# Kernel optimization log

Hardware: AMD Instinct MI355X
Metric: run time of the kernel (lower is better)

Reference implementation:

```python
import jax, jax.numpy as jnp
import numpy as np

H = 2048
B, L, S = 4, 4096, 10

def setup_inputs() -> dict:
    key = jax.random.key(0)
    k1, k2, k3, k4, k5, k6 = jax.random.split(key, 6)
    scale = 1.0 / np.sqrt(H)
    return {
        "h_english": jax.random.normal(k1, (B, L, H), dtype=jnp.float32),
        "h_lojban": jax.random.normal(k2, (B, S, H), dtype=jnp.float32),
        "w_q": jax.random.normal(k3, (H, H), dtype=jnp.float32) * scale,
        "w_k": jax.random.normal(k4, (H, H), dtype=jnp.float32) * scale,
        "w_v": jax.random.normal(k5, (H, H), dtype=jnp.float32) * scale,
        "w_o": jax.random.normal(k6, (H, H), dtype=jnp.float32) * scale,
        "alpha": jnp.float32(0.1),
    }

def reference(h_english, h_lojban, w_q, w_k, w_v, w_o, alpha):
    h = h_english.shape[-1]
    # torch Linear: y = x @ W^T
    q = jnp.einsum('blh,oh->blo', h_english, w_q)   # [B,L,H]
    k = jnp.einsum('bsh,oh->bso', h_lojban, w_k)    # [B,S,H]
    v = jnp.einsum('bsh,oh->bso', h_lojban, w_v)    # [B,S,H]
    scores = jnp.einsum('blh,bsh->bls', q, k) / jnp.sqrt(jnp.float32(h))  # [B,L,S]
    probs = jax.nn.softmax(scores, axis=-1)
    context = jnp.einsum('bls,bsh->blh', probs, v)  # [B,L,H]
    delta = jnp.einsum('blh,oh->blo', context, w_o)
    return h_english + alpha * delta
```

## Files before the change

### kernel.cpp

```cpp
#include <hip/hip_runtime.h>

#define SDIM 10
#define HDIM 2048
#define LDIM 4096
#define BDIM 4

#define KSCALE 0.02209708691207961f

__global__ __launch_bounds__(256) void kv_kernel(
    const float* __restrict__ h_l, const float* __restrict__ w_k,
    const float* __restrict__ w_v, float* __restrict__ k_out,
    float* __restrict__ v_out) {
  const int b = blockIdx.y;
  const int wave = threadIdx.x >> 6;
  const int lane = threadIdx.x & 63;
  const int opair = blockIdx.x * 4 + wave;
  const int o0 = opair * 2;

  const float4* hl4 = (const float4*)(h_l + (size_t)b * SDIM * HDIM);
  const float4* wk0 = (const float4*)(w_k + (size_t)o0 * HDIM);
  const float4* wk1 = (const float4*)(w_k + (size_t)(o0 + 1) * HDIM);
  const float4* wv0 = (const float4*)(w_v + (size_t)o0 * HDIM);
  const float4* wv1 = (const float4*)(w_v + (size_t)(o0 + 1) * HDIM);

  float ak0[SDIM], ak1[SDIM], av0[SDIM], av1[SDIM];
#pragma unroll
  for (int s = 0; s < SDIM; s++) { ak0[s] = ak1[s] = av0[s] = av1[s] = 0.f; }

#pragma unroll
  for (int j = 0; j < 8; j++) {
    const int idx = j * 64 + lane;
    const float4 a0 = wk0[idx], a1 = wk1[idx];
    const float4 c0 = wv0[idx], c1 = wv1[idx];
#pragma unroll
    for (int s = 0; s < SDIM; s++) {
      const float4 h = hl4[s * 512 + idx];
      ak0[s] += a0.x * h.x + a0.y * h.y + a0.z * h.z + a0.w * h.w;
      ak1[s] += a1.x * h.x + a1.y * h.y + a1.z * h.z + a1.w * h.w;
      av0[s] += c0.x * h.x + c0.y * h.y + c0.z * h.z + c0.w * h.w;
      av1[s] += c1.x * h.x + c1.y * h.y + c1.z * h.z + c1.w * h.w;
    }
  }
#pragma unroll
  for (int s = 0; s < SDIM; s++) {
#pragma unroll
    for (int d = 1; d < 64; d <<= 1) {
      ak0[s] += __shfl_xor(ak0[s], d);
      ak1[s] += __shfl_xor(ak1[s], d);
      av0[s] += __shfl_xor(av0[s], d);
      av1[s] += __shfl_xor(av1[s], d);
    }
  }
  if (lane == 0) {
#pragma unroll
    for (int s = 0; s < SDIM; s++) {
      const size_t base = ((size_t)b * SDIM + s) * HDIM + o0;
      k_out[base]     = ak0[s];
      k_out[base + 1] = ak1[s];
      v_out[base]     = av0[s];
      v_out[base + 1] = av1[s];
    }
  }
}

#define OSPLIT 16
__global__ __launch_bounds__(256) void kk_part_kernel(
    const float* __restrict__ k_in, const float* __restrict__ w_q,
    float* __restrict__ part) {
  const int b = blockIdx.z;
  const int oc = blockIdx.y >> 1;
  const int s0 = (blockIdx.y & 1) * 5;
  const int f4 = blockIdx.x * 256 + threadIdx.x;

  __shared__ float ksh[5 * 128];
  for (int idx = threadIdx.x; idx < 5 * 128; idx += 256) {
    const int s = idx >> 7, oo = idx & 127;
    ksh[idx] = k_in[((size_t)b * SDIM + s0 + s) * HDIM + oc * 128 + oo];
  }
  __syncthreads();

  float4 acc[5];
#pragma unroll
  for (int s = 0; s < 5; s++) acc[s] = make_float4(0.f, 0.f, 0.f, 0.f);

  const float4* wq4 = (const float4*)w_q;
  for (int oo = 0; oo < 128; oo++) {
    const float4 w = wq4[(size_t)(oc * 128 + oo) * 512 + f4];
#pragma unroll
    for (int s = 0; s < 5; s++) {
      const float kv = ksh[s * 128 + oo];
      acc[s].x += kv * w.x; acc[s].y += kv * w.y;
      acc[s].z += kv * w.z; acc[s].w += kv * w.w;
    }
  }
#pragma unroll
  for (int s = 0; s < 5; s++) {
    ((float4*)part)[(((size_t)oc * BDIM + b) * SDIM + s0 + s) * 512 + f4] = acc[s];
  }
}

__global__ __launch_bounds__(256) void kk_reduce_kernel(
    const float* __restrict__ part, float* __restrict__ kk_out) {
  const int t = blockIdx.x * 256 + threadIdx.x;
  const float4* p4 = (const float4*)part;
  float4 acc = make_float4(0.f, 0.f, 0.f, 0.f);
#pragma unroll
  for (int p = 0; p < OSPLIT; p++) {
    const float4 v = p4[(size_t)p * 20480 + t];
    acc.x += v.x; acc.y += v.y; acc.z += v.z; acc.w += v.w;
  }
  ((float4*)kk_out)[t] = acc;
}

__global__ __launch_bounds__(256) void vo_kernel(
    const float* __restrict__ v_in, const float* __restrict__ w_o,
    float* __restrict__ vo_out) {
  const int b = blockIdx.y;
  const int wave = threadIdx.x >> 6;
  const int lane = threadIdx.x & 63;
  const int opair = blockIdx.x * 4 + wave;
  const int o0 = opair * 2;

  const float4* vb4 = (const float4*)(v_in + (size_t)b * SDIM * HDIM);
  const float4* wo0 = (const float4*)(w_o + (size_t)o0 * HDIM);
  const float4* wo1 = (const float4*)(w_o + (size_t)(o0 + 1) * HDIM);

  float a0[SDIM], a1[SDIM];
#pragma unroll
  for (int s = 0; s < SDIM; s++) { a0[s] = a1[s] = 0.f; }

#pragma unroll
  for (int j = 0; j < 8; j++) {
    const int idx = j * 64 + lane;
    const float4 w0 = wo0[idx], w1 = wo1[idx];
#pragma unroll
    for (int s = 0; s < SDIM; s++) {
      const float4 h = vb4[s * 512 + idx];
      a0[s] += w0.x * h.x + w0.y * h.y + w0.z * h.z + w0.w * h.w;
      a1[s] += w1.x * h.x + w1.y * h.y + w1.z * h.z + w1.w * h.w;
    }
  }
#pragma unroll
  for (int s = 0; s < SDIM; s++) {
#pragma unroll
    for (int d = 1; d < 64; d <<= 1) {
      a0[s] += __shfl_xor(a0[s], d);
      a1[s] += __shfl_xor(a1[s], d);
    }
  }
  if (lane == 0) {
#pragma unroll
    for (int s = 0; s < SDIM; s++) {
      const size_t base = ((size_t)b * SDIM + s) * HDIM + o0;
      vo_out[base]     = a0[s];
      vo_out[base + 1] = a1[s];
    }
  }
}

__global__ __launch_bounds__(256) void attn_kernel(
    const float* __restrict__ h_e, const float* __restrict__ kk,
    const float* __restrict__ vo, const float* __restrict__ alpha_p,
    float* __restrict__ out) {
  const int b = blockIdx.y;
  const int wave = threadIdx.x >> 6;
  const int lane = threadIdx.x & 63;
  const int tid = threadIdx.x;
  const int row0 = blockIdx.x * 8 + wave * 2;
  const float alpha = *alpha_p;
  const float4* kkb = (const float4*)(kk + (size_t)b * SDIM * HDIM);
  const float4* vob = (const float4*)(vo + (size_t)b * SDIM * HDIM);
  const size_t rowbase = ((size_t)b * LDIM + row0) * HDIM;

  __shared__ float4 lds[SDIM * 128];

  float4 he[2][8];
#pragma unroll
  for (int r = 0; r < 2; r++) {
    const float4* src = (const float4*)(h_e + rowbase + (size_t)r * HDIM);
#pragma unroll
    for (int i = 0; i < 8; i++) he[r][i] = src[i * 64 + lane];
  }

  float acc[2][SDIM];
#pragma unroll
  for (int r = 0; r < 2; r++)
#pragma unroll
    for (int s = 0; s < SDIM; s++) acc[r][s] = 0.f;

  float4 st[5];
#pragma unroll
  for (int k = 0; k < 5; k++) {
    const int idx = k * 256 + tid;
    st[k] = kkb[(idx >> 7) * 512 + (idx & 127)];
  }
#pragma unroll
  for (int j = 0; j < 4; j++) {
    __syncthreads();
#pragma unroll
    for (int k = 0; k < 5; k++) lds[k * 256 + tid] = st[k];
    if (j < 3) {
#pragma unroll
      for (int k = 0; k < 5; k++) {
        const int idx = k * 256 + tid;
        st[k] = kkb[(idx >> 7) * 512 + (j + 1) * 128 + (idx & 127)];
      }
    }
    __syncthreads();
#pragma unroll
    for (int ii = 0; ii < 2; ii++) {
      const int i = j * 2 + ii;
#pragma unroll
      for (int s = 0; s < SDIM; s++) {
        const float4 kv = lds[s * 128 + ii * 64 + lane];
#pragma unroll
        for (int r = 0; r < 2; r++)
          acc[r][s] += he[r][i].x * kv.x + he[r][i].y * kv.y +
                       he[r][i].z * kv.z + he[r][i].w * kv.w;
      }
    }
  }

#pragma unroll
  for (int r = 0; r < 2; r++)
#pragma unroll
    for (int s = 0; s < SDIM; s++) {
      float v = acc[r][s];
      v += __shfl_xor(v, 1);
      v += __shfl_xor(v, 2);
      v += __shfl_xor(v, 4);
      v += __shfl_xor(v, 8);
      v += __shfl_xor(v, 16);
      v += __shfl_xor(v, 32);
      acc[r][s] = v * KSCALE;
    }
#pragma unroll
  for (int r = 0; r < 2; r++) {
    float m = acc[r][0];
#pragma unroll
    for (int s = 1; s < SDIM; s++) m = fmaxf(m, acc[r][s]);
    float sum = 0.f;
#pragma unroll
    for (int s = 0; s < SDIM; s++) {
      acc[r][s] = __expf(acc[r][s] - m);
      sum += acc[r][s];
    }
    const float inv = alpha / sum;
#pragma unroll
    for (int s = 0; s < SDIM; s++) acc[r][s] *= inv;
  }

#pragma unroll
  for (int k = 0; k < 5; k++) {
    const int idx = k * 256 + tid;
    st[k] = vob[(idx >> 7) * 512 + (idx & 127)];
  }
#pragma unroll
  for (int j = 0; j < 4; j++) {
    __syncthreads();
#pragma unroll
    for (int k = 0; k < 5; k++) lds[k * 256 + tid] = st[k];
    if (j < 3) {
#pragma unroll
      for (int k = 0; k < 5; k++) {
        const int idx = k * 256 + tid;
        st[k] = vob[(idx >> 7) * 512 + (j + 1) * 128 + (idx & 127)];
      }
    }
    __syncthreads();
#pragma unroll
    for (int ii = 0; ii < 2; ii++) {
      const int i = j * 2 + ii;
      float4 o4[2];
#pragma unroll
      for (int r = 0; r < 2; r++) o4[r] = he[r][i];
#pragma unroll
      for (int s = 0; s < SDIM; s++) {
        const float4 vv = lds[s * 128 + ii * 64 + lane];
#pragma unroll
        for (int r = 0; r < 2; r++) {
          o4[r].x += acc[r][s] * vv.x;
          o4[r].y += acc[r][s] * vv.y;
          o4[r].z += acc[r][s] * vv.z;
          o4[r].w += acc[r][s] * vv.w;
        }
      }
#pragma unroll
      for (int r = 0; r < 2; r++)
        ((float4*)(out + rowbase + (size_t)r * HDIM))[i * 64 + lane] = o4[r];
    }
  }
}

extern "C" void kernel_launch(void* const* d_in, const int* in_sizes, int n_in,
                              void* d_out, int out_size, void* d_ws, size_t ws_size,
                              hipStream_t stream) {
  const float* h_e   = (const float*)d_in[0];
  const float* h_l   = (const float*)d_in[1];
  const float* w_q   = (const float*)d_in[2];
  const float* w_k   = (const float*)d_in[3];
  const float* w_v   = (const float*)d_in[4];
  const float* w_o   = (const float*)d_in[5];
  const float* alpha = (const float*)d_in[6];
  float* out = (float*)d_out;

  float* ws      = (float*)d_ws;
  float* k_ws    = ws;
  float* v_ws    = ws + 81920;
  float* kk_ws   = ws + 163840;
  float* vo_ws   = ws + 245760;
  float* part_ws = ws + 327680;

  kv_kernel<<<dim3(256, BDIM), 256, 0, stream>>>(h_l, w_k, w_v, k_ws, v_ws);
  kk_part_kernel<<<dim3(2, 32, BDIM), 256, 0, stream>>>(k_ws, w_q, part_ws);
  vo_kernel<<<dim3(256, BDIM), 256, 0, stream>>>(v_ws, w_o, vo_ws);
  kk_reduce_kernel<<<80, 256, 0, stream>>>(part_ws, kk_ws);
  attn_kernel<<<dim3(512, BDIM), 256, 0, stream>>>(h_e, kk_ws, vo_ws, alpha, out);
}
```

Before: 454.7 us.

## Stage projection inputs in LDS and async double-buffer attention operands

The K/V and VO projection kernels now launch one block per output slice and loop over the batch inside the block. Each batch's small activation matrix is staged in shared memory, so all batches reading the same weight rows do so close together in time and the weights are more likely to hit in cache. The attention kernel replaces register-staged copies with direct global-to-LDS async loads into a double buffer. This removes one barrier per chunk, and a launch-bounds hint is added to target occupancy. The costs are larger LDS use, less block-level parallelism in the projection kernels, and a reliance on the barrier to wait for the async LDS loads to finish.

```diff
diff --git a/kernel.cpp b/kernel.cpp
--- a/kernel.cpp
+++ b/kernel.cpp
@@ -11,54 +11,60 @@
     const float* __restrict__ h_l, const float* __restrict__ w_k,
     const float* __restrict__ w_v, float* __restrict__ k_out,
     float* __restrict__ v_out) {
-  const int b = blockIdx.y;
   const int wave = threadIdx.x >> 6;
   const int lane = threadIdx.x & 63;
-  const int opair = blockIdx.x * 4 + wave;
-  const int o0 = opair * 2;
-
-  const float4* hl4 = (const float4*)(h_l + (size_t)b * SDIM * HDIM);
+  const int o0 = blockIdx.x * 8 + wave * 2;
+
+  __shared__ float4 hsh[512 * SDIM];
+
   const float4* wk0 = (const float4*)(w_k + (size_t)o0 * HDIM);
   const float4* wk1 = (const float4*)(w_k + (size_t)(o0 + 1) * HDIM);
   const float4* wv0 = (const float4*)(w_v + (size_t)o0 * HDIM);
   const float4* wv1 = (const float4*)(w_v + (size_t)(o0 + 1) * HDIM);
 
-  float ak0[SDIM], ak1[SDIM], av0[SDIM], av1[SDIM];
-#pragma unroll
-  for (int s = 0; s < SDIM; s++) { ak0[s] = ak1[s] = av0[s] = av1[s] = 0.f; }
-
-#pragma unroll
-  for (int j = 0; j < 8; j++) {
-    const int idx = j * 64 + lane;
-    const float4 a0 = wk0[idx], a1 = wk1[idx];
-    const float4 c0 = wv0[idx], c1 = wv1[idx];
+  for (int b = 0; b < BDIM; b++) {
+    __syncthreads();
+    const float4* src = (const float4*)(h_l + (size_t)b * SDIM * HDIM);
+    for (int i = threadIdx.x; i < 512 * SDIM; i += 256) hsh[i] = src[i];
+    __syncthreads();
+
+    float ak0[SDIM], ak1[SDIM], av0[SDIM], av1[SDIM];
+#pragma unroll
+    for (int s = 0; s < SDIM; s++) { ak0[s] = ak1[s] = av0[s] = av1[s] = 0.f; }
+
+#pragma unroll
+    for (int j = 0; j < 8; j++) {
+      const int idx = j * 64 + lane;
+      const float4 a0 = wk0[idx], a1 = wk1[idx];
+      const float4 c0 = wv0[idx], c1 = wv1[idx];
+#pragma unroll
+      for (int s = 0; s < SDIM; s++) {
+        const float4 h = hsh[s * 512 + idx];
+        ak0[s] += a0.x * h.x + a0.y * h.y + a0.z * h.z + a0.w * h.w;
+        ak1[s] += a1.x * h.x + a1.y * h.y + a1.z * h.z + a1.w * h.w;
+        av0[s] += c0.x * h.x + c0.y * h.y + c0.z * h.z + c0.w * h.w;
+        av1[s] += c1.x * h.x + c1.y * h.y + c1.z * h.z + c1.w * h.w;
+      }
+    }
 #pragma unroll
     for (int s = 0; s < SDIM; s++) {
-      const float4 h = hl4[s * 512 + idx];
-      ak0[s] += a0.x * h.x + a0.y * h.y + a0.z * h.z + a0.w * h.w;
-      ak1[s] += a1.x * h.x + a1.y * h.y + a1.z * h.z + a1.w * h.w;
-      av0[s] += c0.x * h.x + c0.y * h.y + c0.z * h.z + c0.w * h.w;
-      av1[s] += c1.x * h.x + c1.y * h.y + c1.z * h.z + c1.w * h.w;
-    }
-  }
-#pragma unroll
-  for (int s = 0; s < SDIM; s++) {
-#pragma unroll
-    for (int d = 1; d < 64; d <<= 1) {
-      ak0[s] += __shfl_xor(ak0[s], d);
-      ak1[s] += __shfl_xor(ak1[s], d);
-      av0[s] += __shfl_xor(av0[s], d);
-      av1[s] += __shfl_xor(av1[s], d);
-    }
-  }
-  if (lane == 0) {
-#pragma unroll
-    for (int s = 0; s < SDIM; s++) {
-      const size_t base = ((size_t)b * SDIM + s) * HDIM + o0;
-      k_out[base]     = ak0[s];
-      k_out[base + 1] = ak1[s];
-      v_out[base]     = av0[s];
-      v_out[base + 1] = av1[s];
+#pragma unroll
+      for (int d = 1; d < 64; d <<= 1) {
+        ak0[s] += __shfl_xor(ak0[s], d);
+        ak1[s] += __shfl_xor(ak1[s], d);
+        av0[s] += __shfl_xor(av0[s], d);
+        av1[s] += __shfl_xor(av1[s], d);
+      }
+    }
+    if (lane == 0) {
+#pragma unroll
+      for (int s = 0; s < SDIM; s++) {
+        const size_t base = ((size_t)b * SDIM + s) * HDIM + o0;
+        k_out[base]     = ak0[s];
+        k_out[base + 1] = ak1[s];
+        v_out[base]     = av0[s];
+        v_out[base + 1] = av1[s];
+      }
     }
   }
 }
@@ -115,50 +121,70 @@
 __global__ __launch_bounds__(256) void vo_kernel(
     const float* __restrict__ v_in, const float* __restrict__ w_o,
     float* __restrict__ vo_out) {
-  const int b = blockIdx.y;
   const int wave = threadIdx.x >> 6;
   const int lane = threadIdx.x & 63;
-  const int opair = blockIdx.x * 4 + wave;
-  const int o0 = opair * 2;
-
-  const float4* vb4 = (const float4*)(v_in + (size_t)b * SDIM * HDIM);
+  const int o0 = blockIdx.x * 8 + wave * 2;
+
+  __shared__ float4 vsh[512 * SDIM];
+
   const float4* wo0 = (const float4*)(w_o + (size_t)o0 * HDIM);
   const float4* wo1 = (const float4*)(w_o + (size_t)(o0 + 1) * HDIM);
 
-  float a0[SDIM], a1[SDIM];
-#pragma unroll
-  for (int s = 0; s < SDIM; s++) { a0[s] = a1[s] = 0.f; }
-
-#pragma unroll
-  for (int j = 0; j < 8; j++) {
-    const int idx = j * 64 + lane;
-    const float4 w0 = wo0[idx], w1 = wo1[idx];
+  for (int b = 0; b < BDIM; b++) {
+    __syncthreads();
+    const float4* src = (const float4*)(v_in + (size_t)b * SDIM * HDIM);
+    for (int i = threadIdx.x; i < 512 * SDIM; i += 256) vsh[i] = src[i];
+    __syncthreads();
+
+    float a0[SDIM], a1[SDIM];
+#pragma unroll
+    for (int s = 0; s < SDIM; s++) { a0[s] = a1[s] = 0.f; }
+
+#pragma unroll
+    for (int j = 0; j < 8; j++) {
+      const int idx = j * 64 + lane;
+      const float4 w0 = wo0[idx], w1 = wo1[idx];
+#pragma unroll
+      for (int s = 0; s < SDIM; s++) {
+        const float4 h = vsh[s * 512 + idx];
+        a0[s] += w0.x * h.x + w0.y * h.y + w0.z * h.z + w0.w * h.w;
+        a1[s] += w1.x * h.x + w1.y * h.y + w1.z * h.z + w1.w * h.w;
+      }
+    }
 #pragma unroll
     for (int s = 0; s < SDIM; s++) {
-      const float4 h = vb4[s * 512 + idx];
-      a0[s] += w0.x * h.x + w0.y * h.y + w0.z * h.z + w0.w * h.w;
-      a1[s] += w1.x * h.x + w1.y * h.y + w1.z * h.z + w1.w * h.w;
-    }
-  }
-#pragma unroll
-  for (int s = 0; s < SDIM; s++) {
-#pragma unroll
-    for (int d = 1; d < 64; d <<= 1) {
-      a0[s] += __shfl_xor(a0[s], d);
-      a1[s] += __shfl_xor(a1[s], d);
-    }
-  }
-  if (lane == 0) {
-#pragma unroll
-    for (int s = 0; s < SDIM; s++) {
-      const size_t base = ((size_t)b * SDIM + s) * HDIM + o0;
-      vo_out[base]     = a0[s];
-      vo_out[base + 1] = a1[s];
-    }
-  }
-}
-
-__global__ __launch_bounds__(256) void attn_kernel(
+#pragma unroll
+      for (int d = 1; d < 64; d <<= 1) {
+        a0[s] += __shfl_xor(a0[s], d);
+        a1[s] += __shfl_xor(a1[s], d);
+      }
+    }
+    if (lane == 0) {
+#pragma unroll
+      for (int s = 0; s < SDIM; s++) {
+        const size_t base = ((size_t)b * SDIM + s) * HDIM + o0;
+        vo_out[base]     = a0[s];
+        vo_out[base + 1] = a1[s];
+      }
+    }
+  }
+}
+
+__device__ __forceinline__ void stage_chunk(const float4* __restrict__ src,
+                                            float4* lds_base, int j, int tid,
+                                            int wave) {
+#pragma unroll
+  for (int k = 0; k < 5; k++) {
+    const int idx = k * 256 + tid;
+    const float4* g = src + (size_t)(idx >> 7) * 512 + j * 128 + (idx & 127);
+    float4* l = lds_base + k * 256 + (wave << 6);
+    __builtin_amdgcn_global_load_lds(
+        (const __attribute__((address_space(1))) void*)g,
+        (__attribute__((address_space(3))) void*)l, 16, 0, 0);
+  }
+}
+
+__global__ __launch_bounds__(256, 3) void attn_kernel(
     const float* __restrict__ h_e, const float* __restrict__ kk,
     const float* __restrict__ vo, const float* __restrict__ alpha_p,
     float* __restrict__ out) {
@@ -172,7 +198,7 @@
   const float4* vob = (const float4*)(vo + (size_t)b * SDIM * HDIM);
   const size_t rowbase = ((size_t)b * LDIM + row0) * HDIM;
 
-  __shared__ float4 lds[SDIM * 128];
+  __shared__ float4 lds[2][SDIM * 128];
 
   float4 he[2][8];
 #pragma unroll
@@ -188,31 +214,18 @@
 #pragma unroll
     for (int s = 0; s < SDIM; s++) acc[r][s] = 0.f;
 
-  float4 st[5];
-#pragma unroll
-  for (int k = 0; k < 5; k++) {
-    const int idx = k * 256 + tid;
-    st[k] = kkb[(idx >> 7) * 512 + (idx & 127)];
-  }
+  stage_chunk(kkb, lds[0], 0, tid, wave);
 #pragma unroll
   for (int j = 0; j < 4; j++) {
     __syncthreads();
-#pragma unroll
-    for (int k = 0; k < 5; k++) lds[k * 256 + tid] = st[k];
-    if (j < 3) {
-#pragma unroll
-      for (int k = 0; k < 5; k++) {
-        const int idx = k * 256 + tid;
-        st[k] = kkb[(idx >> 7) * 512 + (j + 1) * 128 + (idx & 127)];
-      }
-    }
-    __syncthreads();
+    if (j < 3) stage_chunk(kkb, lds[(j + 1) & 1], j + 1, tid, wave);
+    const float4* buf = lds[j & 1];
 #pragma unroll
     for (int ii = 0; ii < 2; ii++) {
       const int i = j * 2 + ii;
 #pragma unroll
       for (int s = 0; s < SDIM; s++) {
-        const float4 kv = lds[s * 128 + ii * 64 + lane];
+        const float4 kv = buf[s * 128 + ii * 64 + lane];
 #pragma unroll
         for (int r = 0; r < 2; r++)
           acc[r][s] += he[r][i].x * kv.x + he[r][i].y * kv.y +
@@ -250,24 +263,12 @@
     for (int s = 0; s < SDIM; s++) acc[r][s] *= inv;
   }
 
-#pragma unroll
-  for (int k = 0; k < 5; k++) {
-    const int idx = k * 256 + tid;
-    st[k] = vob[(idx >> 7) * 512 + (idx & 127)];
-  }
+  stage_chunk(vob, lds[0], 0, tid, wave);
 #pragma unroll
   for (int j = 0; j < 4; j++) {
     __syncthreads();
-#pragma unroll
-    for (int k = 0; k < 5; k++) lds[k * 256 + tid] = st[k];
-    if (j < 3) {
-#pragma unroll
-      for (int k = 0; k < 5; k++) {
-        const int idx = k * 256 + tid;
-        st[k] = vob[(idx >> 7) * 512 + (j + 1) * 128 + (idx & 127)];
-      }
-    }
-    __syncthreads();
+    if (j < 3) stage_chunk(vob, lds[(j + 1) & 1], j + 1, tid, wave);
+    const float4* buf = lds[j & 1];
 #pragma unroll
     for (int ii = 0; ii < 2; ii++) {
       const int i = j * 2 + ii;
@@ -276,7 +277,7 @@
       for (int r = 0; r < 2; r++) o4[r] = he[r][i];
 #pragma unroll
       for (int s = 0; s < SDIM; s++) {
-        const float4 vv = lds[s * 128 + ii * 64 + lane];
+        const float4 vv = buf[s * 128 + ii * 64 + lane];
 #pragma unroll
         for (int r = 0; r < 2; r++) {
           o4[r].x += acc[r][s] * vv.x;
@@ -311,9 +312,9 @@
   float* vo_ws   = ws + 245760;
   float* part_ws = ws + 327680;
 
-  kv_kernel<<<dim3(256, BDIM), 256, 0, stream>>>(h_l, w_k, w_v, k_ws, v_ws);
+  kv_kernel<<<256, 256, 0, stream>>>(h_l, w_k, w_v, k_ws, v_ws);
   kk_part_kernel<<<dim3(2, 32, BDIM), 256, 0, stream>>>(k_ws, w_q, part_ws);
-  vo_kernel<<<dim3(256, BDIM), 256, 0, stream>>>(v_ws, w_o, vo_ws);
+  vo_kernel<<<256, 256, 0, stream>>>(v_ws, w_o, vo_ws);
   kk_reduce_kernel<<<80, 256, 0, stream>>>(part_ws, kk_ws);
   attn_kernel<<<dim3(512, BDIM), 256, 0, stream>>>(h_e, kk_ws, vo_ws, alpha, out);
 }
```

New measurement: 431.1 us. 1.05x faster.
